# Kernel optimization log

Measured on AMD Instinct MI355X. Metric: run time of the kernel, lower is better.

Reference implementation:

```python
import jax, jax.numpy as jnp
import numpy as np

N, NFEAT, NHID, NCLASS, NHEADS = 4096, 512, 64, 40, 8
ALPHA = 0.2
NEG = -9e15


def setup_inputs() -> dict:
    key = jax.random.key(0)
    ks = jax.random.split(key, 6)
    x = jax.random.normal(ks[0], (N, NFEAT), dtype=jnp.float32)
    adj = jax.random.randint(ks[1], (2, N, N), 0, 2, dtype=jnp.int32)
    # Xavier-ish scaled params
    W1 = jax.random.normal(ks[2], (NHEADS, NFEAT, NHID), dtype=jnp.float32) * (1.0 / np.sqrt(NFEAT))
    a1 = jax.random.normal(ks[3], (NHEADS, 2, NHID), dtype=jnp.float32) * (1.0 / np.sqrt(2 * NHID))
    Wo = jax.random.normal(ks[4], (NHEADS * NHID, NCLASS), dtype=jnp.float32) * (1.0 / np.sqrt(NHEADS * NHID))
    ao = jax.random.normal(ks[5], (2, NCLASS), dtype=jnp.float32) * (1.0 / np.sqrt(2 * NCLASS))
    return {"x": x, "adj": adj, "W1": W1, "a1": a1, "Wo": Wo, "ao": ao}


def _gat_layer(h, adj_mask, W, a_src, a_dst, concat):
    # h: [N,F]; W: [...,F,F']; a_src/a_dst: [...,F']
    if W.ndim == 3:  # multi-head: [H,F,F']
        Wh = jnp.einsum('nf,hfd->hnd', h, W)              # [H,N,F']
        f1 = jnp.einsum('hnd,hd->hn', Wh, a_src)           # [H,N]
        f2 = jnp.einsum('hnd,hd->hn', Wh, a_dst)
        e = jax.nn.leaky_relu(f1[:, :, None] + f2[:, None, :], ALPHA)  # [H,N,N]
        e = jnp.where(adj_mask[None], e, NEG)
        att = jax.nn.softmax(e, axis=-1)
        out = jnp.einsum('hnm,hmd->hnd', att, Wh)          # [H,N,F']
    else:
        Wh = h @ W                                         # [N,F']
        f1 = Wh @ a_src
        f2 = Wh @ a_dst
        e = jax.nn.leaky_relu(f1[:, None] + f2[None, :], ALPHA)
        e = jnp.where(adj_mask, e, NEG)
        att = jax.nn.softmax(e, axis=-1)
        out = att @ Wh
    return jax.nn.elu(out) if concat else out


def reference(x, adj, W1, a1, Wo, ao):
    adj1 = adj[1] > 0
    adj0 = adj[0] > 0
    # layer 1: NHEADS heads, concat=True
    h = _gat_layer(x, adj1, W1, a1[:, 0], a1[:, 1], concat=True)   # [H,N,NHID]
    h = jnp.transpose(h, (1, 0, 2)).reshape(x.shape[0], -1)        # [N, H*NHID]
    # output layer: concat=False, then outer ELU + log_softmax
    out = _gat_layer(h, adj0, Wo, ao[0], ao[1], concat=False)      # [N, NCLASS]
    out = jax.nn.elu(out)
    return jax.nn.log_softmax(out, axis=1)
```

## Files before the change

kernel.cpp:

```cpp
#include <hip/hip_runtime.h>
#include <hip/hip_bf16.h>

#define N      4096
#define NFEAT  512
#define NHID   64
#define NHEADS 8
#define NCLASS 40
#define ALPHA  0.2f
#define LOG2E  1.44269504f

typedef unsigned short u16;
typedef unsigned int   u32;
typedef __attribute__((ext_vector_type(8))) short bf16x8;
typedef __attribute__((ext_vector_type(4))) float f32x4;

__device__ __forceinline__ float b2f(u16 u) {
    return __uint_as_float(((u32)u) << 16);
}
__device__ __forceinline__ u32 rnd_hi(float f) {
    u32 u = __float_as_uint(f);
    return u + 0x7FFFu + ((u >> 16) & 1u);
}
__device__ __forceinline__ u32 pk2(float lo, float hi) {
    __hip_bfloat162 h = __float22bfloat162_rn(make_float2(lo, hi));
    return *(u32*)&h;
}
__device__ __forceinline__ u16 f2b(float f) {
    return (u16)(rnd_hi(f) >> 16);
}
__device__ __forceinline__ float mexp(int m, float t) {
    return m ? __builtin_amdgcn_exp2f(fmaxf(t, ALPHA * t)) : 0.f;
}
__device__ __forceinline__ bf16x8 ones_frag() {
    union { u16 u[8]; bf16x8 v; } o;
    #pragma unroll
    for (int j = 0; j < 8; ++j) o.u[j] = 0x3F80;
    return o.v;
}
__device__ __forceinline__ void gload_lds16(const u16* g, u16* l) {
    __builtin_amdgcn_global_load_lds(
        (const __attribute__((address_space(1))) void*)g,
        (__attribute__((address_space(3))) void*)l,
        16, 0, 0);
}

__global__ __launch_bounds__(256) void kcx(const float* __restrict__ x,
                                           u16* __restrict__ xb) {
    const int g = blockIdx.x * 256 + threadIdx.x;
    const size_t base = (size_t)g * 8;
    float4 v0 = *(const float4*)&x[base];
    float4 v1 = *(const float4*)&x[base + 4];
    uint4 o;
    o.x = pk2(v0.x, v0.y); o.y = pk2(v0.z, v0.w);
    o.z = pk2(v1.x, v1.y); o.w = pk2(v1.z, v1.w);
    *(uint4*)&xb[base] = o;
}

__global__ __launch_bounds__(256) void kcw(const float* __restrict__ W1,
                                           u16* __restrict__ W1b) {
    __shared__ float ts[64 * 68];
    const int t  = threadIdx.x;
    const int f0 = blockIdx.x * 64;
    const int h  = blockIdx.y;
    #pragma unroll
    for (int i = 0; i < 4; ++i) {
        int flat = t + 256 * i;
        int row = flat >> 4;
        int c4  = (flat & 15) * 4;
        *(float4*)&ts[row * 68 + c4] =
            *(const float4*)&W1[((size_t)h * 512 + f0 + row) * 64 + c4];
    }
    __syncthreads();
    const int d  = t >> 2;
    const int fs = (t & 3) * 16;
    u32 p[8];
    #pragma unroll
    for (int j = 0; j < 8; ++j)
        p[j] = pk2(ts[(fs + 2 * j) * 68 + d], ts[(fs + 2 * j + 1) * 68 + d]);
    u32* dst = (u32*)&W1b[((size_t)(h * 64 + d)) * 512 + f0 + fs];
    *(uint4*)dst       = make_uint4(p[0], p[1], p[2], p[3]);
    *(uint4*)(dst + 4) = make_uint4(p[4], p[5], p[6], p[7]);
}

__global__ __launch_bounds__(256, 4) void k1m_gemm1(const u16* __restrict__ xb,
                                                    const u16* __restrict__ W1b,
                                                    const float* __restrict__ a1,
                                                    u16* __restrict__ Wh1T,
                                                    float* __restrict__ F1,
                                                    float* __restrict__ F2) {
    __shared__ __align__(16) u16 xs[2][64 * 64];
    __shared__ __align__(16) u16 wvs[2][64 * 64];
    const int t    = threadIdx.x;
    const int n0   = blockIdx.x * 64;
    const int h    = blockIdx.y;
    const int lane = t & 63;
    const int l15  = lane & 15;
    const int q    = lane >> 4;
    const int wv   = t >> 6;
    const int wrow = wv * 16;
    const int lsub = lane >> 3;
    const int slot = lane & 7;
    const int xb7  = l15 & 7;

    const u16* gx[2];
    const u16* gw[2];
    #pragma unroll
    for (int i = 0; i < 2; ++i) {
        const int r  = wv * 16 + i * 8 + lsub;
        const int sc = (slot ^ lsub) * 8;
        gx[i] = xb  + (size_t)(n0 + r) * 512 + sc;
        gw[i] = W1b + ((size_t)(h * 64 + r)) * 512 + sc;
    }

    f32x4 acc[4];
    #pragma unroll
    for (int df = 0; df < 4; ++df)
        #pragma unroll
        for (int r = 0; r < 4; ++r) acc[df][r] = 0.f;

#define K1_DMA(P, F0)                                                          \
    {                                                                          \
        _Pragma("unroll")                                                      \
        for (int i = 0; i < 2; ++i) {                                          \
            gload_lds16(gx[i] + (F0), &xs[P][(wv * 16 + i * 8) * 64]);         \
            gload_lds16(gw[i] + (F0), &wvs[P][(wv * 16 + i * 8) * 64]);        \
        }                                                                      \
    }
#define K1_MFMA(P)                                                            \
    {                                                                          \
        _Pragma("unroll")                                                      \
        for (int ks = 0; ks < 2; ++ks) {                                       \
            const int sl = ((ks * 4 + q) ^ xb7) * 8;                           \
            bf16x8 a = *(const bf16x8*)&xs[P][(wrow + l15) * 64 + sl];         \
            _Pragma("unroll")                                                  \
            for (int df = 0; df < 4; ++df) {                                   \
                bf16x8 b = *(const bf16x8*)&wvs[P][(df * 16 + l15) * 64 + sl]; \
                acc[df] = __builtin_amdgcn_mfma_f32_16x16x32_bf16(a, b, acc[df], 0, 0, 0); \
            }                                                                  \
        }                                                                      \
    }

    K1_DMA(0, 0)
    __syncthreads();
    for (int f0 = 0; f0 < 512; f0 += 128) {
        K1_DMA(1, f0 + 64)
        K1_MFMA(0)
        __syncthreads();
        if (f0 + 128 < 512)
            K1_DMA(0, f0 + 128)
        K1_MFMA(1)
        __syncthreads();
    }
#undef K1_DMA
#undef K1_MFMA

    #pragma unroll
    for (int df = 0; df < 4; ++df) {
        uint2 o;
        o.x = pk2(acc[df][0], acc[df][1]);
        o.y = pk2(acc[df][2], acc[df][3]);
        *(uint2*)&Wh1T[((size_t)(h * 64 + df * 16 + l15)) * 4096 + n0 + wrow + q * 4] = o;
    }
    float a1v[4], a2v[4];
    #pragma unroll
    for (int df = 0; df < 4; ++df) {
        a1v[df] = a1[h * 128 + df * 16 + l15];
        a2v[df] = a1[h * 128 + 64 + df * 16 + l15];
    }
    #pragma unroll
    for (int r = 0; r < 4; ++r) {
        float s1 = 0.f, s2 = 0.f;
        #pragma unroll
        for (int df = 0; df < 4; ++df) {
            s1 += acc[df][r] * a1v[df];
            s2 += acc[df][r] * a2v[df];
        }
        #pragma unroll
        for (int off = 8; off >= 1; off >>= 1) {
            s1 += __shfl_xor(s1, off);
            s2 += __shfl_xor(s2, off);
        }
        if (l15 == 0) {
            int n = n0 + wrow + q * 4 + r;
            F1[h * 4096 + n] = s1 * LOG2E;
            F2[h * 4096 + n] = s2 * LOG2E;
        }
    }
}

__global__ __launch_bounds__(256, 4) void k3_attn1(const int* __restrict__ adj1,
                                                   const u16* __restrict__ Wh1T,
                                                   const float* __restrict__ F1,
                                                   const float* __restrict__ F2,
                                                   float* __restrict__ h1) {
    __shared__ __align__(16) u16 wbf[2][32 * 72];
    __shared__ __align__(16) u16 whT[2][64 * 64];
    __shared__ float zs[32];
    const int t    = threadIdx.x;
    const int n0   = blockIdx.x * 32;
    const int h    = blockIdx.y;
    const int lane = t & 63;
    const int l15  = lane & 15;
    const int q    = lane >> 4;
    const int wv   = t >> 6;
    const int rb   = (wv & 1) * 16;
    const int dh   = wv >> 1;
    const int rg2  = t >> 4;
    const int c4h  = (t & 15) * 4;
    const bf16x8 bones = ones_frag();

    const float f1a = F1[h * N + n0 + rg2];
    const float f1b = F1[h * N + n0 + rg2 + 16];

    const int lsub = lane >> 3;
    const int slot = lane & 7;
    const u16* gsrc[2];
    #pragma unroll
    for (int i = 0; i < 2; ++i) {
        const int r = wv * 16 + i * 8 + lsub;
        gsrc[i] = Wh1T + ((size_t)(h * 64 + r)) * 4096 + (slot ^ lsub) * 8;
    }
    const int xb7 = l15 & 7;

    const int*   adjA = adj1 + (size_t)(n0 + rg2) * N + c4h;
    const int*   adjB = adj1 + (size_t)(n0 + rg2 + 16) * N + c4h;
    const float* f2p  = F2 + (size_t)h * N + c4h;

    f32x4 accd[2], accz;
    #pragma unroll
    for (int j = 0; j < 2; ++j)
        #pragma unroll
        for (int r = 0; r < 4; ++r) accd[j][r] = 0.f;
    #pragma unroll
    for (int r = 0; r < 4; ++r) accz[r] = 0.f;

    int4   ajA0 = *(const int4*)(adjA);
    int4   ajB0 = *(const int4*)(adjB);
    float4 f2r0 = *(const float4*)(f2p);
    #pragma unroll
    for (int i = 0; i < 2; ++i)
        gload_lds16(gsrc[i], &whT[0][(wv * 16 + i * 8) * 64]);
    int4   ajA1 = *(const int4*)(adjA + 64);
    int4   ajB1 = *(const int4*)(adjB + 64);
    float4 f2r1 = *(const float4*)(f2p + 64);
    {
        uint2 pa, pb;
        pa.x = pk2(mexp(ajA0.x, f1a + f2r0.x), mexp(ajA0.y, f1a + f2r0.y));
        pa.y = pk2(mexp(ajA0.z, f1a + f2r0.z), mexp(ajA0.w, f1a + f2r0.w));
        pb.x = pk2(mexp(ajB0.x, f1b + f2r0.x), mexp(ajB0.y, f1b + f2r0.y));
        pb.y = pk2(mexp(ajB0.z, f1b + f2r0.z), mexp(ajB0.w, f1b + f2r0.w));
        *(uint2*)&wbf[0][rg2 * 72 + c4h]        = pa;
        *(uint2*)&wbf[0][(rg2 + 16) * 72 + c4h] = pb;
    }
    __syncthreads();

    int mh = 0;
#define K3_STEP(RP, MGA, MGB, MGF, PFA, PFB, PFF)                               \
    {                                                                           \
        const int mh1 = (mh + 64) & 4095;                                       \
        const int mh2 = (mh + 128) & 4095;                                      \
        _Pragma("unroll")                                                       \
        for (int i = 0; i < 2; ++i)                                             \
            gload_lds16(gsrc[i] + mh1, &whT[(RP) ^ 1][(wv * 16 + i * 8) * 64]); \
        int4 a4 = MGA; int4 b4 = MGB; float4 fv = MGF;                          \
        PFA = *(const int4*)(adjA + mh2);                                       \
        PFB = *(const int4*)(adjB + mh2);                                       \
        PFF = *(const float4*)(f2p + mh2);                                      \
        uint2 pa, pb;                                                           \
        pa.x = pk2(mexp(a4.x, f1a + fv.x), mexp(a4.y, f1a + fv.y));             \
        pa.y = pk2(mexp(a4.z, f1a + fv.z), mexp(a4.w, f1a + fv.w));             \
        pb.x = pk2(mexp(b4.x, f1b + fv.x), mexp(b4.y, f1b + fv.y));             \
        pb.y = pk2(mexp(b4.z, f1b + fv.z), mexp(b4.w, f1b + fv.w));             \
        *(uint2*)&wbf[(RP) ^ 1][rg2 * 72 + c4h]        = pa;                    \
        *(uint2*)&wbf[(RP) ^ 1][(rg2 + 16) * 72 + c4h] = pb;                    \
        _Pragma("unroll")                                                       \
        for (int ks = 0; ks < 2; ++ks) {                                        \
            bf16x8 a = *(const bf16x8*)&wbf[RP][(rb + l15) * 72 + ks * 32 + q * 8]; \
            _Pragma("unroll")                                                   \
            for (int j = 0; j < 2; ++j) {                                       \
                bf16x8 b = *(const bf16x8*)                                     \
                    &whT[RP][((dh * 2 + j) * 16 + l15) * 64 + (((ks * 4 + q) ^ xb7) * 8)]; \
                accd[j] = __builtin_amdgcn_mfma_f32_16x16x32_bf16(a, b, accd[j], 0, 0, 0); \
            }                                                                   \
            if (dh == 0)                                                        \
                accz = __builtin_amdgcn_mfma_f32_16x16x32_bf16(a, bones, accz, 0, 0, 0); \
        }                                                                       \
        __syncthreads();                                                        \
        mh = mh1;                                                               \
    }

    for (int it = 0; it < 32; ++it) {
        K3_STEP(0, ajA1, ajB1, f2r1, ajA0, ajB0, f2r0)
        K3_STEP(1, ajA0, ajB0, f2r0, ajA1, ajB1, f2r1)
    }
#undef K3_STEP

    if (dh == 0 && l15 == 0) {
        #pragma unroll
        for (int r = 0; r < 4; ++r) zs[rb + q * 4 + r] = accz[r];
    }
    __syncthreads();
    #pragma unroll
    for (int r = 0; r < 4; ++r) {
        const int nl = rb + q * 4 + r;
        const float z = fmaxf(zs[nl], 1e-30f);
        #pragma unroll
        for (int j = 0; j < 2; ++j) {
            float v = accd[j][r] / z;
            v = v > 0.f ? v : __expf(v) - 1.f;
            h1[(size_t)(n0 + nl) * 512 + h * 64 + (dh * 2 + j) * 16 + l15] = v;
        }
    }
}

__global__ __launch_bounds__(256) void k4_gemm2(const float* __restrict__ h1,
                                                const float* __restrict__ Wo,
                                                const float* __restrict__ ao,
                                                float* __restrict__ F1o,
                                                float* __restrict__ F2o,
                                                u16* __restrict__ Wh2T) {
    const int t = threadIdx.x;
    const int c = t & 63;
    const int n = blockIdx.x * 4 + (t >> 6);
    float acc = 0.f;
    if (c < NCLASS) {
        const float* hrow = &h1[(size_t)n * 512];
        #pragma unroll 8
        for (int f = 0; f < 512; ++f)
            acc += hrow[f] * Wo[f * NCLASS + c];
        Wh2T[(size_t)c * 4096 + n] = f2b(acc);
    }
    float s1 = (c < NCLASS) ? acc * ao[c] : 0.f;
    float s2 = (c < NCLASS) ? acc * ao[NCLASS + c] : 0.f;
    #pragma unroll
    for (int off = 32; off >= 1; off >>= 1) {
        s1 += __shfl_xor(s1, off);
        s2 += __shfl_xor(s2, off);
    }
    if (c == 0) {
        F1o[n] = s1 * LOG2E;
        F2o[n] = s2 * LOG2E;
    }
}

__global__ __launch_bounds__(256, 5) void k5a_attn2(const int* __restrict__ adj0,
                                                    const u16* __restrict__ Wh2T,
                                                    const float* __restrict__ F1o,
                                                    const float* __restrict__ F2o,
                                                    float* __restrict__ pacc,
                                                    float* __restrict__ pz) {
    __shared__ __align__(16) u16 wbf[64 * 136];
    __shared__ __align__(16) u16 whT[48 * 128];
    __shared__ float f1s[64];
    const int t     = threadIdx.x;
    const int n0    = blockIdx.x * 64;
    const int chunk = blockIdx.y;
    const int mbase = chunk * 256;
    const int lane  = t & 63;
    const int l15   = lane & 15;
    const int q     = lane >> 4;
    const int wrow  = (t >> 6) * 16;
    const int c4    = (t & 31) * 4;
    const int rg    = t >> 5;
    const bf16x8 bones = ones_frag();
    if (t < 64) f1s[t] = F1o[n0 + t];
    #pragma unroll
    for (int i = 0; i < 4; ++i)
        whT[40 * 128 + t + 256 * i] = 0;

    const int wv   = t >> 6;
    const int lsub = lane >> 4;
    const int slot = lane & 15;
    const int ninst = (wv < 2) ? 4 : ((wv == 2) ? 2 : 0);
    const u16* gsrc[4];
    #pragma unroll
    for (int i = 0; i < 4; ++i) {
        int row_l = wv * 16 + i * 4 + lsub;
        int rl    = (row_l < 40) ? row_l : 0;
        int sc    = (slot ^ ((i * 4 + lsub) & 7)) * 8;
        gsrc[i] = Wh2T + (size_t)rl * 4096 + sc;
    }
    u16* ldst = &whT[wv * 2048];
    const int xb7 = l15 & 7;

    f32x4 acc[4];
    #pragma unroll
    for (int df = 0; df < 4; ++df)
        #pragma unroll
        for (int r = 0; r < 4; ++r) acc[df][r] = 0.f;

    int4 aprev[8];
    #pragma unroll
    for (int i = 0; i < 8; ++i)
        aprev[i] = *(const int4*)&adj0[(size_t)(n0 + rg + 8 * i) * N + mbase + c4];
    __syncthreads();

    #pragma unroll
    for (int mt = 0; mt < 2; ++mt) {
        const int m0 = mbase + mt * 128;
        #pragma unroll
        for (int i = 0; i < 4; ++i)
            if (i < ninst)
                gload_lds16(gsrc[i] + m0, ldst + i * 512);
        float4 F2v = *(const float4*)&F2o[m0 + c4];
        #pragma unroll
        for (int i = 0; i < 8; ++i) {
            int rr = rg + 8 * i;
            int4 a4 = aprev[i];
            float f1v = f1s[rr];
            float w0 = mexp(a4.x, f1v + F2v.x);
            float w1 = mexp(a4.y, f1v + F2v.y);
            float w2 = mexp(a4.z, f1v + F2v.z);
            float w3 = mexp(a4.w, f1v + F2v.w);
            uint2 pk;
            pk.x = pk2(w0, w1);
            pk.y = pk2(w2, w3);
            *(uint2*)&wbf[rr * 136 + c4] = pk;
        }
        int mn = mbase + ((mt + 1) & 1) * 128;
        #pragma unroll
        for (int i = 0; i < 8; ++i)
            aprev[i] = *(const int4*)&adj0[(size_t)(n0 + rg + 8 * i) * N + mn + c4];
        __syncthreads();
        #pragma unroll
        for (int ks = 0; ks < 4; ++ks) {
            int k0 = ks * 32 + q * 8;
            bf16x8 a = *(const bf16x8*)&wbf[(wrow + l15) * 136 + k0];
            #pragma unroll
            for (int df = 0; df < 3; ++df) {
                bf16x8 b = *(const bf16x8*)
                    &whT[(df * 16 + l15) * 128 + (((ks * 4 + q) ^ xb7) * 8)];
                acc[df] = __builtin_amdgcn_mfma_f32_16x16x32_bf16(a, b, acc[df], 0, 0, 0);
            }
            acc[3] = __builtin_amdgcn_mfma_f32_16x16x32_bf16(a, bones, acc[3], 0, 0, 0);
        }
        __syncthreads();
    }
    #pragma unroll
    for (int r = 0; r < 4; ++r) {
        int n = n0 + wrow + q * 4 + r;
        if (l15 == 0) pz[(size_t)chunk * N + n] = acc[3][r];
        #pragma unroll
        for (int df = 0; df < 3; ++df) {
            int c = df * 16 + l15;
            if (c < NCLASS)
                pacc[((size_t)chunk * N + n) * NCLASS + c] = acc[df][r];
        }
    }
}

__global__ __launch_bounds__(256) void k5b_final(const float* __restrict__ pacc,
                                                 const float* __restrict__ pz,
                                                 float* __restrict__ out) {
    const int t = threadIdx.x;
    const int lane = t & 63;
    const int n = blockIdx.x * 4 + (t >> 6);
    float s = 0.f, Z = 0.f;
    #pragma unroll
    for (int ch = 0; ch < 16; ++ch) {
        Z += pz[(size_t)ch * N + n];
        if (lane < NCLASS) s += pacc[(size_t)(ch * N + n) * NCLASS + lane];
    }
    float v;
    if (lane < NCLASS) {
        v = s / fmaxf(Z, 1e-30f);
        v = v > 0.f ? v : __expf(v) - 1.f;
    } else {
        v = -INFINITY;
    }
    float mx = v;
    #pragma unroll
    for (int off = 32; off >= 1; off >>= 1) mx = fmaxf(mx, __shfl_xor(mx, off));
    float ex = (lane < NCLASS) ? __expf(v - mx) : 0.f;
    #pragma unroll
    for (int off = 32; off >= 1; off >>= 1) ex += __shfl_xor(ex, off);
    float lse = mx + __logf(ex);
    if (lane < NCLASS) out[(size_t)n * NCLASS + lane] = v - lse;
}

extern "C" void kernel_launch(void* const* d_in, const int* in_sizes, int n_in,
                              void* d_out, int out_size, void* d_ws, size_t ws_size,
                              hipStream_t stream) {
    const float* x   = (const float*)d_in[0];
    const int*   adj = (const int*)d_in[1];
    const float* W1  = (const float*)d_in[2];
    const float* a1  = (const float*)d_in[3];
    const float* Wo  = (const float*)d_in[4];
    const float* ao  = (const float*)d_in[5];

    float* ws    = (float*)d_ws;
    float* h1    = ws;
    float* F1    = h1 + 2097152;
    float* F2    = F1 + 32768;
    float* F1o   = F2 + 32768;
    float* F2o   = F1o + 4096;
    float* pz    = F2o + 4096;
    float* pz1   = pz + 65536;
    u16*   Wh1T  = (u16*)(pz1 + 65536);
    u16*   Wh2T  = Wh1T + 2097152;
    float* R     = (float*)(Wh2T + 163840);
    u16*   xb    = (u16*)R;
    u16*   W1b   = xb + 2097152;
    float* pacc  = R;

    const int* adj0 = adj;
    const int* adj1 = adj + (size_t)N * N;

    hipLaunchKernelGGL(kcx,       dim3(1024),   dim3(256), 0, stream, x, xb);
    hipLaunchKernelGGL(kcw,       dim3(8, 8),   dim3(256), 0, stream, W1, W1b);
    hipLaunchKernelGGL(k1m_gemm1, dim3(64, 8),  dim3(256), 0, stream, xb, W1b, a1, Wh1T, F1, F2);
    hipLaunchKernelGGL(k3_attn1,  dim3(128, 8), dim3(256), 0, stream, adj1, Wh1T, F1, F2, h1);
    hipLaunchKernelGGL(k4_gemm2,  dim3(1024),   dim3(256), 0, stream, h1, Wo, ao, F1o, F2o, Wh2T);
    hipLaunchKernelGGL(k5a_attn2, dim3(64, 16), dim3(256), 0, stream, adj0, Wh2T, F1o, F2o, pacc, pz);
    hipLaunchKernelGGL(k5b_final, dim3(1024),   dim3(256), 0, stream, pacc, pz, (float*)d_out);
}
```

Before: 308.8 us.

## Deepen adjacency prefetch and use partial vmcnt wait before barrier

Prefetches the adjacency and F2 register tiles three steps ahead instead of two, and replaces __syncthreads in the main attention loop with an explicit s_waitcnt vmcnt(3) plus raw s_barrier. The goal is to keep in-flight global register loads outstanding across the barrier, so only the LDS-direct Wh tile loads must finish, which hides HBM latency for the adjacency stream. The risk is correctness: it relies on the vmcnt ordering assumption holding for the queued loads. It also keeps more registers live.

```diff
diff --git a/kernel.cpp b/kernel.cpp
--- a/kernel.cpp
+++ b/kernel.cpp
@@ -234,38 +234,41 @@
     #pragma unroll
     for (int r = 0; r < 4; ++r) accz[r] = 0.f;
 
-    int4   ajA0 = *(const int4*)(adjA);
-    int4   ajB0 = *(const int4*)(adjB);
-    float4 f2r0 = *(const float4*)(f2p);
+    int4   tA = *(const int4*)(adjA);
+    int4   tB = *(const int4*)(adjB);
+    float4 tF = *(const float4*)(f2p);
     #pragma unroll
     for (int i = 0; i < 2; ++i)
         gload_lds16(gsrc[i], &whT[0][(wv * 16 + i * 8) * 64]);
-    int4   ajA1 = *(const int4*)(adjA + 64);
-    int4   ajB1 = *(const int4*)(adjB + 64);
-    float4 f2r1 = *(const float4*)(f2p + 64);
+    int4   aA1 = *(const int4*)(adjA + 64);
+    int4   aB1 = *(const int4*)(adjB + 64);
+    float4 f21 = *(const float4*)(f2p + 64);
+    int4   aA0 = *(const int4*)(adjA + 128);
+    int4   aB0 = *(const int4*)(adjB + 128);
+    float4 f20 = *(const float4*)(f2p + 128);
     {
         uint2 pa, pb;
-        pa.x = pk2(mexp(ajA0.x, f1a + f2r0.x), mexp(ajA0.y, f1a + f2r0.y));
-        pa.y = pk2(mexp(ajA0.z, f1a + f2r0.z), mexp(ajA0.w, f1a + f2r0.w));
-        pb.x = pk2(mexp(ajB0.x, f1b + f2r0.x), mexp(ajB0.y, f1b + f2r0.y));
-        pb.y = pk2(mexp(ajB0.z, f1b + f2r0.z), mexp(ajB0.w, f1b + f2r0.w));
+        pa.x = pk2(mexp(tA.x, f1a + tF.x), mexp(tA.y, f1a + tF.y));
+        pa.y = pk2(mexp(tA.z, f1a + tF.z), mexp(tA.w, f1a + tF.w));
+        pb.x = pk2(mexp(tB.x, f1b + tF.x), mexp(tB.y, f1b + tF.y));
+        pb.y = pk2(mexp(tB.z, f1b + tF.z), mexp(tB.w, f1b + tF.w));
         *(uint2*)&wbf[0][rg2 * 72 + c4h]        = pa;
         *(uint2*)&wbf[0][(rg2 + 16) * 72 + c4h] = pb;
     }
     __syncthreads();
 
     int mh = 0;
-#define K3_STEP(RP, MGA, MGB, MGF, PFA, PFB, PFF)                               \
+#define K3_STEP(RP, SA, SB, SF)                                                 \
     {                                                                           \
         const int mh1 = (mh + 64) & 4095;                                       \
-        const int mh2 = (mh + 128) & 4095;                                      \
+        const int mh3 = (mh + 192) & 4095;                                      \
         _Pragma("unroll")                                                       \
         for (int i = 0; i < 2; ++i)                                             \
             gload_lds16(gsrc[i] + mh1, &whT[(RP) ^ 1][(wv * 16 + i * 8) * 64]); \
-        int4 a4 = MGA; int4 b4 = MGB; float4 fv = MGF;                          \
-        PFA = *(const int4*)(adjA + mh2);                                       \
-        PFB = *(const int4*)(adjB + mh2);                                       \
-        PFF = *(const float4*)(f2p + mh2);                                      \
+        int4 a4 = SA; int4 b4 = SB; float4 fv = SF;                             \
+        SA = *(const int4*)(adjA + mh3);                                        \
+        SB = *(const int4*)(adjB + mh3);                                        \
+        SF = *(const float4*)(f2p + mh3);                                       \
         uint2 pa, pb;                                                           \
         pa.x = pk2(mexp(a4.x, f1a + fv.x), mexp(a4.y, f1a + fv.y));             \
         pa.y = pk2(mexp(a4.z, f1a + fv.z), mexp(a4.w, f1a + fv.w));             \
@@ -285,16 +288,20 @@
             if (dh == 0)                                                        \
                 accz = __builtin_amdgcn_mfma_f32_16x16x32_bf16(a, bones, accz, 0, 0, 0); \
         }                                                                       \
-        __syncthreads();                                                        \
+        asm volatile("s_waitcnt vmcnt(3) lgkmcnt(0)" ::: "memory");             \
+        __builtin_amdgcn_sched_barrier(0);                                      \
+        __builtin_amdgcn_s_barrier();                                           \
+        __builtin_amdgcn_sched_barrier(0);                                      \
         mh = mh1;                                                               \
     }
 
     for (int it = 0; it < 32; ++it) {
-        K3_STEP(0, ajA1, ajB1, f2r1, ajA0, ajB0, f2r0)
-        K3_STEP(1, ajA0, ajB0, f2r0, ajA1, ajB1, f2r1)
+        K3_STEP(0, aA1, aB1, f21)
+        K3_STEP(1, aA0, aB0, f20)
     }
 #undef K3_STEP
 
+    __syncthreads();
     if (dh == 0 && l15 == 0) {
         #pragma unroll
         for (int r = 0; r < 4; ++r) zs[rb + q * 4 + r] = accz[r];
```

Result: no change. 312.3 us (+1.1%).

## Halve attention row tile to 16 rows, raise occupancy, deepen adjacency prefetch

Applied to the files above, without the earlier changes.

The first-layer attention kernel now processes 16 query rows per block instead of 32, with each wave owning one 16-column slice of the head dimension. The grid doubles and launch bounds rise to 7 blocks per CU, so fewer registers are used and more waves are resident to hide latency on the adjacency stream. Adjacency and F2 prefetch now runs three steps ahead instead of two. The cost is that each Wh1T tile loaded into LDS is reused by half as many rows, which doubles total Wh1T traffic.

```diff
diff --git a/kernel.cpp b/kernel.cpp
--- a/kernel.cpp
+++ b/kernel.cpp
@@ -188,29 +188,26 @@
     }
 }
 
-__global__ __launch_bounds__(256, 4) void k3_attn1(const int* __restrict__ adj1,
+__global__ __launch_bounds__(256, 7) void k3_attn1(const int* __restrict__ adj1,
                                                    const u16* __restrict__ Wh1T,
                                                    const float* __restrict__ F1,
                                                    const float* __restrict__ F2,
                                                    float* __restrict__ h1) {
-    __shared__ __align__(16) u16 wbf[2][32 * 72];
+    __shared__ __align__(16) u16 wbf[2][16 * 72];
     __shared__ __align__(16) u16 whT[2][64 * 64];
-    __shared__ float zs[32];
+    __shared__ float zs[16];
     const int t    = threadIdx.x;
-    const int n0   = blockIdx.x * 32;
+    const int n0   = blockIdx.x * 16;
     const int h    = blockIdx.y;
     const int lane = t & 63;
     const int l15  = lane & 15;
     const int q    = lane >> 4;
     const int wv   = t >> 6;
-    const int rb   = (wv & 1) * 16;
-    const int dh   = wv >> 1;
-    const int rg2  = t >> 4;
+    const int rg1  = t >> 4;
     const int c4h  = (t & 15) * 4;
     const bf16x8 bones = ones_frag();
 
-    const float f1a = F1[h * N + n0 + rg2];
-    const float f1b = F1[h * N + n0 + rg2 + 16];
+    const float f1v = F1[h * N + n0 + rg1];
 
     const int lsub = lane >> 3;
     const int slot = lane & 7;
@@ -222,67 +219,52 @@
     }
     const int xb7 = l15 & 7;
 
-    const int*   adjA = adj1 + (size_t)(n0 + rg2) * N + c4h;
-    const int*   adjB = adj1 + (size_t)(n0 + rg2 + 16) * N + c4h;
+    const int*   adjp = adj1 + (size_t)(n0 + rg1) * N + c4h;
     const float* f2p  = F2 + (size_t)h * N + c4h;
 
-    f32x4 accd[2], accz;
-    #pragma unroll
-    for (int j = 0; j < 2; ++j)
-        #pragma unroll
-        for (int r = 0; r < 4; ++r) accd[j][r] = 0.f;
-    #pragma unroll
-    for (int r = 0; r < 4; ++r) accz[r] = 0.f;
-
-    int4   ajA0 = *(const int4*)(adjA);
-    int4   ajB0 = *(const int4*)(adjB);
-    float4 f2r0 = *(const float4*)(f2p);
+    f32x4 accd, accz;
+    #pragma unroll
+    for (int r = 0; r < 4; ++r) { accd[r] = 0.f; accz[r] = 0.f; }
+
+    int4   tA  = *(const int4*)(adjp);
+    float4 tF  = *(const float4*)(f2p);
     #pragma unroll
     for (int i = 0; i < 2; ++i)
         gload_lds16(gsrc[i], &whT[0][(wv * 16 + i * 8) * 64]);
-    int4   ajA1 = *(const int4*)(adjA + 64);
-    int4   ajB1 = *(const int4*)(adjB + 64);
-    float4 f2r1 = *(const float4*)(f2p + 64);
+    int4   s1a = *(const int4*)(adjp + 64);
+    float4 s1f = *(const float4*)(f2p + 64);
+    int4   s0a = *(const int4*)(adjp + 128);
+    float4 s0f = *(const float4*)(f2p + 128);
     {
-        uint2 pa, pb;
-        pa.x = pk2(mexp(ajA0.x, f1a + f2r0.x), mexp(ajA0.y, f1a + f2r0.y));
-        pa.y = pk2(mexp(ajA0.z, f1a + f2r0.z), mexp(ajA0.w, f1a + f2r0.w));
-        pb.x = pk2(mexp(ajB0.x, f1b + f2r0.x), mexp(ajB0.y, f1b + f2r0.y));
-        pb.y = pk2(mexp(ajB0.z, f1b + f2r0.z), mexp(ajB0.w, f1b + f2r0.w));
-        *(uint2*)&wbf[0][rg2 * 72 + c4h]        = pa;
-        *(uint2*)&wbf[0][(rg2 + 16) * 72 + c4h] = pb;
+        uint2 pa;
+        pa.x = pk2(mexp(tA.x, f1v + tF.x), mexp(tA.y, f1v + tF.y));
+        pa.y = pk2(mexp(tA.z, f1v + tF.z), mexp(tA.w, f1v + tF.w));
+        *(uint2*)&wbf[0][rg1 * 72 + c4h] = pa;
     }
     __syncthreads();
 
     int mh = 0;
-#define K3_STEP(RP, MGA, MGB, MGF, PFA, PFB, PFF)                               \
+#define K3_STEP(RP, SA, SF)                                                     \
     {                                                                           \
         const int mh1 = (mh + 64) & 4095;                                       \
-        const int mh2 = (mh + 128) & 4095;                                      \
+        const int mh3 = (mh + 192) & 4095;                                      \
         _Pragma("unroll")                                                       \
         for (int i = 0; i < 2; ++i)                                             \
             gload_lds16(gsrc[i] + mh1, &whT[(RP) ^ 1][(wv * 16 + i * 8) * 64]); \
-        int4 a4 = MGA; int4 b4 = MGB; float4 fv = MGF;                          \
-        PFA = *(const int4*)(adjA + mh2);                                       \
-        PFB = *(const int4*)(adjB + mh2);                                       \
-        PFF = *(const float4*)(f2p + mh2);                                      \
-        uint2 pa, pb;                                                           \
-        pa.x = pk2(mexp(a4.x, f1a + fv.x), mexp(a4.y, f1a + fv.y));             \
-        pa.y = pk2(mexp(a4.z, f1a + fv.z), mexp(a4.w, f1a + fv.w));             \
-        pb.x = pk2(mexp(b4.x, f1b + fv.x), mexp(b4.y, f1b + fv.y));             \
-        pb.y = pk2(mexp(b4.z, f1b + fv.z), mexp(b4.w, f1b + fv.w));             \
-        *(uint2*)&wbf[(RP) ^ 1][rg2 * 72 + c4h]        = pa;                    \
-        *(uint2*)&wbf[(RP) ^ 1][(rg2 + 16) * 72 + c4h] = pb;                    \
+        int4 a4 = SA; float4 fv = SF;                                           \
+        SA = *(const int4*)(adjp + mh3);                                        \
+        SF = *(const float4*)(f2p + mh3);                                       \
+        uint2 pa;                                                               \
+        pa.x = pk2(mexp(a4.x, f1v + fv.x), mexp(a4.y, f1v + fv.y));             \
+        pa.y = pk2(mexp(a4.z, f1v + fv.z), mexp(a4.w, f1v + fv.w));             \
+        *(uint2*)&wbf[(RP) ^ 1][rg1 * 72 + c4h] = pa;                           \
         _Pragma("unroll")                                                       \
         for (int ks = 0; ks < 2; ++ks) {                                        \
-            bf16x8 a = *(const bf16x8*)&wbf[RP][(rb + l15) * 72 + ks * 32 + q * 8]; \
-            _Pragma("unroll")                                                   \
-            for (int j = 0; j < 2; ++j) {                                       \
-                bf16x8 b = *(const bf16x8*)                                     \
-                    &whT[RP][((dh * 2 + j) * 16 + l15) * 64 + (((ks * 4 + q) ^ xb7) * 8)]; \
-                accd[j] = __builtin_amdgcn_mfma_f32_16x16x32_bf16(a, b, accd[j], 0, 0, 0); \
-            }                                                                   \
-            if (dh == 0)                                                        \
+            bf16x8 a = *(const bf16x8*)&wbf[RP][l15 * 72 + ks * 32 + q * 8];    \
+            bf16x8 b = *(const bf16x8*)                                         \
+                &whT[RP][(wv * 16 + l15) * 64 + (((ks * 4 + q) ^ xb7) * 8)];    \
+            accd = __builtin_amdgcn_mfma_f32_16x16x32_bf16(a, b, accd, 0, 0, 0); \
+            if (wv == 0)                                                        \
                 accz = __builtin_amdgcn_mfma_f32_16x16x32_bf16(a, bones, accz, 0, 0, 0); \
         }                                                                       \
         __syncthreads();                                                        \
@@ -290,26 +272,23 @@
     }
 
     for (int it = 0; it < 32; ++it) {
-        K3_STEP(0, ajA1, ajB1, f2r1, ajA0, ajB0, f2r0)
-        K3_STEP(1, ajA0, ajB0, f2r0, ajA1, ajB1, f2r1)
+        K3_STEP(0, s1a, s1f)
+        K3_STEP(1, s0a, s0f)
     }
 #undef K3_STEP
 
-    if (dh == 0 && l15 == 0) {
-        #pragma unroll
-        for (int r = 0; r < 4; ++r) zs[rb + q * 4 + r] = accz[r];
+    if (wv == 0 && l15 == 0) {
+        #pragma unroll
+        for (int r = 0; r < 4; ++r) zs[q * 4 + r] = accz[r];
     }
     __syncthreads();
     #pragma unroll
     for (int r = 0; r < 4; ++r) {
-        const int nl = rb + q * 4 + r;
+        const int nl = q * 4 + r;
         const float z = fmaxf(zs[nl], 1e-30f);
-        #pragma unroll
-        for (int j = 0; j < 2; ++j) {
-            float v = accd[j][r] / z;
-            v = v > 0.f ? v : __expf(v) - 1.f;
-            h1[(size_t)(n0 + nl) * 512 + h * 64 + (dh * 2 + j) * 16 + l15] = v;
-        }
+        float v = accd[r] / z;
+        v = v > 0.f ? v : __expf(v) - 1.f;
+        h1[(size_t)(n0 + nl) * 512 + h * 64 + wv * 16 + l15] = v;
     }
 }
 
@@ -509,7 +488,7 @@
     hipLaunchKernelGGL(kcx,       dim3(1024),   dim3(256), 0, stream, x, xb);
     hipLaunchKernelGGL(kcw,       dim3(8, 8),   dim3(256), 0, stream, W1, W1b);
     hipLaunchKernelGGL(k1m_gemm1, dim3(64, 8),  dim3(256), 0, stream, xb, W1b, a1, Wh1T, F1, F2);
-    hipLaunchKernelGGL(k3_attn1,  dim3(128, 8), dim3(256), 0, stream, adj1, Wh1T, F1, F2, h1);
+    hipLaunchKernelGGL(k3_attn1,  dim3(256, 8), dim3(256), 0, stream, adj1, Wh1T, F1, F2, h1);
     hipLaunchKernelGGL(k4_gemm2,  dim3(1024),   dim3(256), 0, stream, h1, Wo, ao, F1o, F2o, Wh2T);
     hipLaunchKernelGGL(k5a_attn2, dim3(64, 16), dim3(256), 0, stream, adj0, Wh2T, F1o, F2o, pacc, pz);
     hipLaunchKernelGGL(k5b_final, dim3(1024),   dim3(256), 0, stream, pacc, pz, (float*)d_out);
```

Result: slower. 350.7 us (+13.6%).
